# Kernel tuning notes

Measured on AMD Instinct MI355X. Metric: run time of the kernel, lower is better.

## Reference

```python
import jax, jax.numpy as jnp
import numpy as np

MAT_MODE = ((0, 1), (0, 2), (1, 2))
VEC_MODE = (2, 1, 0)


def _bilinear2d(feat, xy):
    # feat [C,H,W]; xy [N,2] in [-1,1], x indexes W, y indexes H (align_corners=True)
    C, H, W = feat.shape
    x = jnp.clip((xy[:, 0] + 1.0) * 0.5 * (W - 1), 0.0, W - 1)
    y = jnp.clip((xy[:, 1] + 1.0) * 0.5 * (H - 1), 0.0, H - 1)
    x0 = jnp.floor(x).astype(jnp.int32)
    y0 = jnp.floor(y).astype(jnp.int32)
    x1 = jnp.minimum(x0 + 1, W - 1)
    y1 = jnp.minimum(y0 + 1, H - 1)
    wx = (x - x0)[None, :]
    wy = (y - y0)[None, :]
    f00 = feat[:, y0, x0]
    f01 = feat[:, y0, x1]
    f10 = feat[:, y1, x0]
    f11 = feat[:, y1, x1]
    top = f00 * (1.0 - wx) + f01 * wx
    bot = f10 * (1.0 - wx) + f11 * wx
    return top * (1.0 - wy) + bot * wy  # [C,N]


def _linear1d(feat, z):
    # feat [C,L]; z [N] in [-1,1] (align_corners=True); x-coord of grid_sample is 0 (width=1)
    C, L = feat.shape
    y = jnp.clip((z + 1.0) * 0.5 * (L - 1), 0.0, L - 1)
    y0 = jnp.floor(y).astype(jnp.int32)
    y1 = jnp.minimum(y0 + 1, L - 1)
    wy = (y - y0)[None, :]
    return feat[:, y0] * (1.0 - wy) + feat[:, y1] * wy  # [C,N]


def _skew(w):
    # w [N,3] -> [N,3,3]
    z = jnp.zeros_like(w[:, 0])
    return jnp.stack([
        jnp.stack([z, -w[:, 2], w[:, 1]], -1),
        jnp.stack([w[:, 2], z, -w[:, 0]], -1),
        jnp.stack([-w[:, 1], w[:, 0], z], -1),
    ], axis=1)


def _sample_bwfield(planes, lines, xn):
    # planes [3,6,16,H,W], lines [3,6,16,L], xn [N,3] normalized -> bwf [N,6]
    N = xn.shape[0]
    bwf = jnp.zeros((6, N), dtype=xn.dtype)
    for p in range(3):
        m0, m1 = MAT_MODE[p]
        xy = jnp.stack([xn[:, m0], xn[:, m1]], axis=-1)  # [N,2]
        S, C, H, W = planes[p].shape  # 6,16,H,W
        psamp = _bilinear2d(planes[p].reshape(S * C, H, W), xy).reshape(S, C, N)
        lsamp = _linear1d(lines[p].reshape(S * C, -1), xn[:, VEC_MODE[p]]).reshape(S, C, N)
        bwf = bwf + jnp.sum(psamp * lsamp, axis=1)  # [6,N]
    return bwf.T  # [N,6]


def _warp(xyz, viewdirs, planes, lines, ray_aabb):
    shape = xyz.shape
    pts = xyz.reshape(-1, 3)
    inv = 2.0 / (ray_aabb[1] - ray_aabb[0])
    xn = (pts - ray_aabb[0]) * inv - 1.0
    bwf = _sample_bwfield(planes, lines, xn)  # [N,6]
    w, v = bwf[:, :3], bwf[:, 3:]
    theta = jnp.sqrt(jnp.clip(jnp.sum(w * w, axis=-1), 1e-6, None))  # [N]
    w = w / theta[:, None]
    v = v / theta[:, None]
    Wm = _skew(w)                                   # [N,3,3]
    W2 = jnp.einsum('nij,njk->nik', Wm, Wm)
    s = jnp.sin(theta)[:, None, None]
    c = jnp.cos(theta)[:, None, None]
    th = theta[:, None, None]
    I = jnp.eye(3, dtype=xyz.dtype)
    R = I + s * Wm + (1.0 - c) * W2                 # exp_so3
    P = th * I + (1.0 - c) * Wm + (th - s) * W2     # V(theta)
    t = jnp.einsum('nij,nj->ni', P, v)              # translation
    xw = jnp.einsum('nij,nj->ni', R, pts) + t
    vw = jnp.einsum('nij,nj->ni', R, viewdirs.reshape(-1, 3))
    return xw.reshape(shape), vw.reshape(shape)


def setup_inputs() -> dict:
    key = jax.random.key(0)
    k1, k2, k3, k4 = jax.random.split(key, 4)
    n_rays, n_samp = 2048, 256
    G = 128
    xyz = jax.random.uniform(k1, (n_rays, n_samp, 3), jnp.float32, -1.4, 1.4)
    vd = jax.random.normal(k2, (n_rays, n_samp, 3), jnp.float32)
    vd = vd / jnp.linalg.norm(vd, axis=-1, keepdims=True)
    planes = 0.1 * jax.random.normal(k3, (3, 6, 16, G, G), jnp.float32)
    lines = 0.1 * jax.random.normal(k4, (3, 6, 16, G), jnp.float32)
    ray_aabb = jnp.array([[-1.5, -1.5, -1.5], [1.5, 1.5, 1.5]], jnp.float32)
    transforms = jnp.zeros((4, 4), jnp.float32)
    ray_valid = jnp.ones((n_rays, n_samp), bool)
    return {"xyz_sampled": xyz, "viewdirs": vd, "transforms": transforms,
            "ray_valid": ray_valid, "planes": planes, "lines": lines,
            "ray_aabb": ray_aabb}


def reference(xyz_sampled, viewdirs, transforms, ray_valid, planes, lines, ray_aabb):
    # transforms and ray_valid are accepted but unused by Map_BWCaster.forward
    return _warp(xyz_sampled, viewdirs, planes, lines, ray_aabb)
```

## Files before the change

kernel.cpp:

```cpp
#include <hip/hip_runtime.h>
#include <cstdint>
#include <cstddef>

#define GRES 128
#define SC   96

typedef float v2f __attribute__((ext_vector_type(2)));

template<bool HI>
__device__ __forceinline__ v2f cvt2(uint32_t q)
{
    return __builtin_amdgcn_cvt_pk_f32_fp8(q, HI);
}

__device__ __forceinline__ uint32_t u4w(const uint4& q, int c)
{
    return c == 0 ? q.x : c == 1 ? q.y : c == 2 ? q.z : q.w;
}

#define NPLANE_T (3 * 12 * GRES * GRES)
#define NLINE_T  (3 * 12 * GRES)

__global__ __launch_bounds__(256) void tp_split(const float* __restrict__ planes,
                                                const float* __restrict__ lines,
                                                uint8_t* __restrict__ A,
                                                uint8_t* __restrict__ B,
                                                uint8_t* __restrict__ L)
{
    int t = blockIdx.x * 256 + threadIdx.x;
    if (t < NPLANE_T) {
        int xy = t & (GRES * GRES - 1);
        int pg = t >> 14;
        int g  = pg % 12;
        int p  = pg / 12;
        int ch0 = 8 * g;
        const float* src = planes + ((size_t)(p * SC + ch0) * (GRES * GRES)) + xy;
        float v[8];
        #pragma unroll
        for (int i = 0; i < 8; ++i) v[i] = src[(size_t)i * (GRES * GRES)];
        uint32_t w0 = 0, w1 = 0;
        w0 = __builtin_amdgcn_cvt_pk_fp8_f32(v[0], v[1], w0, false);
        w0 = __builtin_amdgcn_cvt_pk_fp8_f32(v[2], v[3], w0, true);
        w1 = __builtin_amdgcn_cvt_pk_fp8_f32(v[4], v[5], w1, false);
        w1 = __builtin_amdgcn_cvt_pk_fp8_f32(v[6], v[7], w1, true);
        uint2 pkt = make_uint2(w0, w1);
        int texel = (p << 14) + xy;
        if (g < 8)
            *(uint2*)(A + (size_t)texel * 64 + 8 * g) = pkt;
        else
            *(uint2*)(B + (size_t)texel * 32 + 8 * (g - 8)) = pkt;
    } else if (t < NPLANE_T + NLINE_T) {
        int r = t - NPLANE_T;
        int z  = r & (GRES - 1);
        int pg = r >> 7;
        int g  = pg % 12;
        int p  = pg / 12;
        int ch0 = 8 * g;
        const float* src = lines + ((size_t)(p * SC + ch0) * GRES) + z;
        float v[8];
        #pragma unroll
        for (int i = 0; i < 8; ++i) v[i] = src[(size_t)i * GRES];
        uint32_t w0 = 0, w1 = 0;
        w0 = __builtin_amdgcn_cvt_pk_fp8_f32(v[0], v[1], w0, false);
        w0 = __builtin_amdgcn_cvt_pk_fp8_f32(v[2], v[3], w0, true);
        w1 = __builtin_amdgcn_cvt_pk_fp8_f32(v[4], v[5], w1, false);
        w1 = __builtin_amdgcn_cvt_pk_fp8_f32(v[6], v[7], w1, true);
        *(uint2*)(L + (size_t)(p * GRES + z) * 128 + 8 * g) = make_uint2(w0, w1);
    }
}

__device__ __forceinline__ void axis_setup(float xnv, int& i0, int& i1, float& w)
{
    float f = (xnv + 1.0f) * 0.5f * (float)(GRES - 1);
    f = fminf(fmaxf(f, 0.0f), (float)(GRES - 1));
    float ff = floorf(f);
    i0 = (int)ff;
    i1 = min(i0 + 1, GRES - 1);
    w  = f - ff;
}

__global__ __launch_bounds__(256) void bwcast_s4(
    const float* __restrict__ xyz, const float* __restrict__ vdirs,
    const uint8_t* __restrict__ A, const uint8_t* __restrict__ B,
    const uint8_t* __restrict__ L, const float* __restrict__ aabb,
    float* __restrict__ out, int N)
{
    int t = blockIdx.x * 256 + threadIdx.x;
    int n = t >> 2;
    int l = t & 3;
    if (n >= N) return;
    int lane = threadIdx.x & 63;

    float px = xyz[3 * n + 0], py = xyz[3 * n + 1], pz = xyz[3 * n + 2];
    float xn[3];
    xn[0] = (px - aabb[0]) * (2.0f / (aabb[3] - aabb[0])) - 1.0f;
    xn[1] = (py - aabb[1]) * (2.0f / (aabb[4] - aabb[1])) - 1.0f;
    xn[2] = (pz - aabb[2]) * (2.0f / (aabb[5] - aabb[2])) - 1.0f;

    uint32_t aoff[3][4], boff[3][4];
    uint32_t lo4[3][2], lo2[3][2];
    float W[3][4], UZ[3], WZ[3];

    #pragma unroll
    for (int p = 0; p < 3; ++p) {
        constexpr int M0[3] = {0, 0, 1};
        constexpr int M1[3] = {1, 2, 2};
        constexpr int MV[3] = {2, 1, 0};
        int x0, x1, y0, y1, z0, z1;
        float wx, wy, wz;
        axis_setup(xn[M0[p]], x0, x1, wx);
        axis_setup(xn[M1[p]], y0, y1, wy);
        axis_setup(xn[MV[p]], z0, z1, wz);
        uint32_t t00 = (uint32_t)((p * GRES + y0) * GRES + x0);
        uint32_t t01 = (uint32_t)((p * GRES + y0) * GRES + x1);
        uint32_t t10 = (uint32_t)((p * GRES + y1) * GRES + x0);
        uint32_t t11 = (uint32_t)((p * GRES + y1) * GRES + x1);
        uint32_t a16 = (uint32_t)l * 16u, b8 = (uint32_t)l * 8u;
        aoff[p][0] = t00 * 64u + a16;  boff[p][0] = t00 * 32u + b8;
        aoff[p][1] = t01 * 64u + a16;  boff[p][1] = t01 * 32u + b8;
        aoff[p][2] = t10 * 64u + a16;  boff[p][2] = t10 * 32u + b8;
        aoff[p][3] = t11 * 64u + a16;  boff[p][3] = t11 * 32u + b8;
        uint32_t r0 = (uint32_t)(p * GRES + z0) * 128u;
        uint32_t r1 = (uint32_t)(p * GRES + z1) * 128u;
        lo4[p][0] = r0 + a16;          lo2[p][0] = r0 + 64u + b8;
        lo4[p][1] = r1 + a16;          lo2[p][1] = r1 + 64u + b8;
        W[p][0] = (1.f - wx) * (1.f - wy);
        W[p][1] = wx * (1.f - wy);
        W[p][2] = (1.f - wx) * wy;
        W[p][3] = wx * wy;
        UZ[p] = 1.f - wz;
        WZ[p] = wz;
    }

    v2f aLE = (v2f)(0.f), aLO = (v2f)(0.f);
    v2f aHE = (v2f)(0.f), aHO = (v2f)(0.f);

    #pragma unroll
    for (int p = 0; p < 3; ++p) {
        uint4 a4[4]; uint2 b2[4];
        #pragma unroll
        for (int c = 0; c < 4; ++c) {
            a4[c] = *(const uint4*)(A + aoff[p][c]);
            b2[c] = *(const uint2*)(B + boff[p][c]);
        }
        uint4 l4[2]; uint2 l2[2];
        #pragma unroll
        for (int d = 0; d < 2; ++d) {
            l4[d] = *(const uint4*)(L + lo4[p][d]);
            l2[d] = *(const uint2*)(L + lo2[p][d]);
        }
        v2f w0v = (v2f)(W[p][0]);
        v2f w1v = (v2f)(W[p][1]);
        v2f w2v = (v2f)(W[p][2]);
        v2f w3v = (v2f)(W[p][3]);
        v2f uzv = (v2f)(UZ[p]);
        v2f wzv = (v2f)(WZ[p]);

        #pragma unroll
        for (int k = 0; k < 4; ++k) {
            uint32_t wa0 = u4w(a4[0], k), wa1 = u4w(a4[1], k);
            uint32_t wa2 = u4w(a4[2], k), wa3 = u4w(a4[3], k);
            uint32_t wl0 = u4w(l4[0], k), wl1 = u4w(l4[1], k);
            v2f pv = cvt2<false>(wa0) * w0v;
            pv = cvt2<false>(wa1) * w1v + pv;
            pv = cvt2<false>(wa2) * w2v + pv;
            pv = cvt2<false>(wa3) * w3v + pv;
            v2f lv = cvt2<false>(wl1) * wzv;
            lv = cvt2<false>(wl0) * uzv + lv;
            aLE = pv * lv + aLE;
            v2f pu = cvt2<true>(wa0) * w0v;
            pu = cvt2<true>(wa1) * w1v + pu;
            pu = cvt2<true>(wa2) * w2v + pu;
            pu = cvt2<true>(wa3) * w3v + pu;
            v2f lu = cvt2<true>(wl1) * wzv;
            lu = cvt2<true>(wl0) * uzv + lu;
            aLO = pu * lu + aLO;
        }
        #pragma unroll
        for (int k = 0; k < 2; ++k) {
            uint32_t wb0 = k ? b2[0].y : b2[0].x;
            uint32_t wb1 = k ? b2[1].y : b2[1].x;
            uint32_t wb2 = k ? b2[2].y : b2[2].x;
            uint32_t wb3 = k ? b2[3].y : b2[3].x;
            uint32_t wl0 = k ? l2[0].y : l2[0].x;
            uint32_t wl1 = k ? l2[1].y : l2[1].x;
            v2f pv = cvt2<false>(wb0) * w0v;
            pv = cvt2<false>(wb1) * w1v + pv;
            pv = cvt2<false>(wb2) * w2v + pv;
            pv = cvt2<false>(wb3) * w3v + pv;
            v2f lv = cvt2<false>(wl1) * wzv;
            lv = cvt2<false>(wl0) * uzv + lv;
            aHE = pv * lv + aHE;
            v2f pu = cvt2<true>(wb0) * w0v;
            pu = cvt2<true>(wb1) * w1v + pu;
            pu = cvt2<true>(wb2) * w2v + pu;
            pu = cvt2<true>(wb3) * w3v + pu;
            v2f lu = cvt2<true>(wl1) * wzv;
            lu = cvt2<true>(wl0) * uzv + lu;
            aHO = pu * lu + aHO;
        }
    }

    v2f sl = aLE + aLO;
    float part_lo = sl[0] + sl[1];
    v2f sh = aHE + aHO;
    float part_hi = sh[0] + sh[1];

    int base = lane & ~3;
    float bw[6];
    bw[0] = __shfl(part_lo, base + 0);
    bw[1] = __shfl(part_lo, base + 1);
    bw[2] = __shfl(part_lo, base + 2);
    bw[3] = __shfl(part_lo, base + 3);
    float ph2 = part_hi + __shfl_xor(part_hi, 1);
    bw[4] = __shfl(ph2, base + 0);
    bw[5] = __shfl(ph2, base + 2);

    float wxr = bw[0], wyr = bw[1], wzr = bw[2];
    float dotw = wxr * wxr + wyr * wyr + wzr * wzr;
    float theta = sqrtf(fmaxf(dotw, 1e-6f));
    float it = 1.0f / theta;
    float ux = wxr * it, uy = wyr * it, un = wzr * it;
    float vx = bw[3] * it, vy = bw[4] * it, vz = bw[5] * it;
    float st, ct;
    sincosf(theta, &st, &ct);
    float q   = ux * ux + uy * uy + un * un;
    float omc = 1.0f - ct;
    float ra = 1.0f - omc * q;
    float R00 = ra + omc * ux * ux;
    float R01 = omc * ux * uy - st * un;
    float R02 = omc * ux * un + st * uy;
    float R10 = omc * uy * ux + st * un;
    float R11 = ra + omc * uy * uy;
    float R12 = omc * uy * un - st * ux;
    float R20 = omc * un * ux - st * uy;
    float R21 = omc * un * uy + st * ux;
    float R22 = ra + omc * un * un;
    float tms = theta - st;
    float pa  = theta - tms * q;
    float P00 = pa + tms * ux * ux;
    float P01 = tms * ux * uy - omc * un;
    float P02 = tms * ux * un + omc * uy;
    float P10 = tms * uy * ux + omc * un;
    float P11 = pa + tms * uy * uy;
    float P12 = tms * uy * un - omc * ux;
    float P20 = tms * un * ux - omc * uy;
    float P21 = tms * un * uy + omc * ux;
    float P22 = pa + tms * un * un;

    float tx = P00 * vx + P01 * vy + P02 * vz;
    float ty = P10 * vx + P11 * vy + P12 * vz;
    float tz = P20 * vx + P21 * vy + P22 * vz;

    float ox = R00 * px + R01 * py + R02 * pz + tx;
    float oy = R10 * px + R11 * py + R12 * pz + ty;
    float oz = R20 * px + R21 * py + R22 * pz + tz;

    float dx = vdirs[3 * n + 0], dy = vdirs[3 * n + 1], dz = vdirs[3 * n + 2];
    float wvx = R00 * dx + R01 * dy + R02 * dz;
    float wvy = R10 * dx + R11 * dy + R12 * dz;
    float wvz = R20 * dx + R21 * dy + R22 * dz;

    if (l < 3) {
        float o  = (l == 0) ? ox : (l == 1) ? oy : oz;
        float wv = (l == 0) ? wvx : (l == 1) ? wvy : wvz;
        out[3 * n + l] = o;
        out[(size_t)3 * N + 3 * n + l] = wv;
    }
}

__global__ __launch_bounds__(256) void bwcast_direct(
    const float* __restrict__ xyz, const float* __restrict__ vdirs,
    const float* __restrict__ PL, const float* __restrict__ LN,
    const float* __restrict__ aabb, float* __restrict__ out, int N)
{
    int n = blockIdx.x * 256 + threadIdx.x;
    if (n >= N) return;

    float px = xyz[3 * n + 0], py = xyz[3 * n + 1], pz = xyz[3 * n + 2];
    float xn[3];
    xn[0] = (px - aabb[0]) * (2.0f / (aabb[3] - aabb[0])) - 1.0f;
    xn[1] = (py - aabb[1]) * (2.0f / (aabb[4] - aabb[1])) - 1.0f;
    xn[2] = (pz - aabb[2]) * (2.0f / (aabb[5] - aabb[2])) - 1.0f;

    float bw[6] = {0.f, 0.f, 0.f, 0.f, 0.f, 0.f};

    #pragma unroll
    for (int p = 0; p < 3; ++p) {
        constexpr int M0[3] = {0, 0, 1};
        constexpr int M1[3] = {1, 2, 2};
        constexpr int MV[3] = {2, 1, 0};
        int x0, x1, y0, y1, z0, z1;
        float wx, wy, wz;
        axis_setup(xn[M0[p]], x0, x1, wx);
        axis_setup(xn[M1[p]], y0, y1, wy);
        axis_setup(xn[MV[p]], z0, z1, wz);
        float w00 = (1.f - wx) * (1.f - wy);
        float w01 = wx * (1.f - wy);
        float w10 = (1.f - wx) * wy;
        float w11 = wx * wy;
        float uz = 1.f - wz;
        #pragma unroll
        for (int s = 0; s < 6; ++s) {
            float acc = bw[s];
            for (int c = 0; c < 16; ++c) {
                int sc = s * 16 + c;
                const float* pb = PL + (size_t)(p * SC + sc) * (GRES * GRES);
                float f00 = pb[y0 * GRES + x0];
                float f01 = pb[y0 * GRES + x1];
                float f10 = pb[y1 * GRES + x0];
                float f11 = pb[y1 * GRES + x1];
                const float* lb = LN + (size_t)(p * SC + sc) * GRES;
                float lv = fmaf(lb[z0], uz, lb[z1] * wz);
                float pv = fmaf(f00, w00, fmaf(f01, w01, fmaf(f10, w10, f11 * w11)));
                acc = fmaf(pv, lv, acc);
            }
            bw[s] = acc;
        }
    }

    float wxr = bw[0], wyr = bw[1], wzr = bw[2];
    float dotw = wxr * wxr + wyr * wyr + wzr * wzr;
    float theta = sqrtf(fmaxf(dotw, 1e-6f));
    float it = 1.0f / theta;
    float ux = wxr * it, uy = wyr * it, un = wzr * it;
    float vx = bw[3] * it, vy = bw[4] * it, vz = bw[5] * it;
    float st, ct;
    sincosf(theta, &st, &ct);
    float q   = ux * ux + uy * uy + un * un;
    float omc = 1.0f - ct;
    float ra = 1.0f - omc * q;
    float R00 = ra + omc * ux * ux;
    float R01 = omc * ux * uy - st * un;
    float R02 = omc * ux * un + st * uy;
    float R10 = omc * uy * ux + st * un;
    float R11 = ra + omc * uy * uy;
    float R12 = omc * uy * un - st * ux;
    float R20 = omc * un * ux - st * uy;
    float R21 = omc * un * uy + st * ux;
    float R22 = ra + omc * un * un;
    float tms = theta - st;
    float pa  = theta - tms * q;
    float P00 = pa + tms * ux * ux;
    float P01 = tms * ux * uy - omc * un;
    float P02 = tms * ux * un + omc * uy;
    float P10 = tms * uy * ux + omc * un;
    float P11 = pa + tms * uy * uy;
    float P12 = tms * uy * un - omc * ux;
    float P20 = tms * un * ux - omc * uy;
    float P21 = tms * un * uy + omc * ux;
    float P22 = pa + tms * un * un;

    float tx = P00 * vx + P01 * vy + P02 * vz;
    float ty = P10 * vx + P11 * vy + P12 * vz;
    float tz = P20 * vx + P21 * vy + P22 * vz;

    out[3 * n + 0] = R00 * px + R01 * py + R02 * pz + tx;
    out[3 * n + 1] = R10 * px + R11 * py + R12 * pz + ty;
    out[3 * n + 2] = R20 * px + R21 * py + R22 * pz + tz;

    float dx = vdirs[3 * n + 0], dy = vdirs[3 * n + 1], dz = vdirs[3 * n + 2];
    size_t off = (size_t)3 * N;
    out[off + 3 * n + 0] = R00 * dx + R01 * dy + R02 * dz;
    out[off + 3 * n + 1] = R10 * dx + R11 * dy + R12 * dz;
    out[off + 3 * n + 2] = R20 * dx + R21 * dy + R22 * dz;
}

extern "C" void kernel_launch(void* const* d_in, const int* in_sizes, int n_in,
                              void* d_out, int out_size, void* d_ws, size_t ws_size,
                              hipStream_t stream)
{
    const float* xyz    = (const float*)d_in[0];
    const float* vd     = (const float*)d_in[1];
    const float* planes = (const float*)d_in[4];
    const float* lines  = (const float*)d_in[5];
    const float* aabb   = (const float*)d_in[6];
    float* out = (float*)d_out;

    int N = in_sizes[0] / 3;

    size_t szA = (size_t)3 * GRES * GRES * 64;
    size_t szB = (size_t)3 * GRES * GRES * 32;
    size_t szL = (size_t)3 * GRES * 128;

    if (ws_size >= szA + szB + szL) {
        uint8_t* A = (uint8_t*)d_ws;
        uint8_t* Bp = A + szA;
        uint8_t* L = Bp + szB;
        int tp_threads = NPLANE_T + NLINE_T;
        tp_split<<<(tp_threads + 255) / 256, 256, 0, stream>>>(planes, lines, A, Bp, L);
        int threads = N * 4;
        bwcast_s4<<<(threads + 255) / 256, 256, 0, stream>>>(
            xyz, vd, A, Bp, L, aabb, out, N);
    } else {
        bwcast_direct<<<(N + 255) / 256, 256, 0, stream>>>(xyz, vd, planes, lines, aabb, out, N);
    }
}
```

Before: 155.5 us.

## Split each point across two lanes instead of four with wider fp8 loads

Each sample point is now handled by two threads instead of four, and each thread loads 32 bytes of A, 16 of B, and matching line bytes per corner. The six bw components are exchanged with three xor-shuffles, and each lane writes one of the two outputs. Accurate sincosf is replaced by __sinf/__cosf. This halves the thread count and the redundant per-point setup and epilogue math, at the cost of more registers per thread and possibly lower occupancy and memory-level parallelism.

Measured after the change: 181.5 us. +16.8%, slower.

```diff
diff --git a/kernel.cpp b/kernel.cpp
--- a/kernel.cpp
+++ b/kernel.cpp
@@ -79,17 +79,38 @@
     w  = f - ff;
 }
 
-__global__ __launch_bounds__(256) void bwcast_s4(
+__device__ __forceinline__ void word_fma(
+    uint32_t wa0, uint32_t wa1, uint32_t wa2, uint32_t wa3,
+    uint32_t wl0, uint32_t wl1,
+    v2f w0v, v2f w1v, v2f w2v, v2f w3v, v2f uzv, v2f wzv,
+    v2f& accE, v2f& accO)
+{
+    v2f pv = cvt2<false>(wa0) * w0v;
+    pv = cvt2<false>(wa1) * w1v + pv;
+    pv = cvt2<false>(wa2) * w2v + pv;
+    pv = cvt2<false>(wa3) * w3v + pv;
+    v2f lv = cvt2<false>(wl1) * wzv;
+    lv = cvt2<false>(wl0) * uzv + lv;
+    accE = pv * lv + accE;
+    v2f pu = cvt2<true>(wa0) * w0v;
+    pu = cvt2<true>(wa1) * w1v + pu;
+    pu = cvt2<true>(wa2) * w2v + pu;
+    pu = cvt2<true>(wa3) * w3v + pu;
+    v2f lu = cvt2<true>(wl1) * wzv;
+    lu = cvt2<true>(wl0) * uzv + lu;
+    accO = pu * lu + accO;
+}
+
+__global__ __launch_bounds__(256) void bwcast_d2(
     const float* __restrict__ xyz, const float* __restrict__ vdirs,
     const uint8_t* __restrict__ A, const uint8_t* __restrict__ B,
     const uint8_t* __restrict__ L, const float* __restrict__ aabb,
     float* __restrict__ out, int N)
 {
     int t = blockIdx.x * 256 + threadIdx.x;
-    int n = t >> 2;
-    int l = t & 3;
+    int n = t >> 1;
+    int h = t & 1;
     if (n >= N) return;
-    int lane = threadIdx.x & 63;
 
     float px = xyz[3 * n + 0], py = xyz[3 * n + 1], pz = xyz[3 * n + 2];
     float xn[3];
@@ -97,9 +118,12 @@
     xn[1] = (py - aabb[1]) * (2.0f / (aabb[4] - aabb[1])) - 1.0f;
     xn[2] = (pz - aabb[2]) * (2.0f / (aabb[5] - aabb[2])) - 1.0f;
 
-    uint32_t aoff[3][4], boff[3][4];
-    uint32_t lo4[3][2], lo2[3][2];
-    float W[3][4], UZ[3], WZ[3];
+    const uint32_t a32 = (uint32_t)h * 32u;
+    const uint32_t b16 = (uint32_t)h * 16u;
+
+    v2f acA0E = (v2f)(0.f), acA0O = (v2f)(0.f);
+    v2f acA1E = (v2f)(0.f), acA1O = (v2f)(0.f);
+    v2f acBE  = (v2f)(0.f), acBO  = (v2f)(0.f);
 
     #pragma unroll
     for (int p = 0; p < 3; ++p) {
@@ -111,110 +135,168 @@
         axis_setup(xn[M0[p]], x0, x1, wx);
         axis_setup(xn[M1[p]], y0, y1, wy);
         axis_setup(xn[MV[p]], z0, z1, wz);
-        uint32_t t00 = (uint32_t)((p * GRES + y0) * GRES + x0);
-        uint32_t t01 = (uint32_t)((p * GRES + y0) * GRES + x1);
-        uint32_t t10 = (uint32_t)((p * GRES + y1) * GRES + x0);
-        uint32_t t11 = (uint32_t)((p * GRES + y1) * GRES + x1);
-        uint32_t a16 = (uint32_t)l * 16u, b8 = (uint32_t)l * 8u;
-        aoff[p][0] = t00 * 64u + a16;  boff[p][0] = t00 * 32u + b8;
-        aoff[p][1] = t01 * 64u + a16;  boff[p][1] = t01 * 32u + b8;
-        aoff[p][2] = t10 * 64u + a16;  boff[p][2] = t10 * 32u + b8;
-        aoff[p][3] = t11 * 64u + a16;  boff[p][3] = t11 * 32u + b8;
+        uint32_t tex[4];
+        tex[0] = (uint32_t)((p * GRES + y0) * GRES + x0);
+        tex[1] = (uint32_t)((p * GRES + y0) * GRES + x1);
+        tex[2] = (uint32_t)((p * GRES + y1) * GRES + x0);
+        tex[3] = (uint32_t)((p * GRES + y1) * GRES + x1);
         uint32_t r0 = (uint32_t)(p * GRES + z0) * 128u;
         uint32_t r1 = (uint32_t)(p * GRES + z1) * 128u;
-        lo4[p][0] = r0 + a16;          lo2[p][0] = r0 + 64u + b8;
-        lo4[p][1] = r1 + a16;          lo2[p][1] = r1 + 64u + b8;
-        W[p][0] = (1.f - wx) * (1.f - wy);
-        W[p][1] = wx * (1.f - wy);
-        W[p][2] = (1.f - wx) * wy;
-        W[p][3] = wx * wy;
-        UZ[p] = 1.f - wz;
-        WZ[p] = wz;
-    }
-
-    v2f aLE = (v2f)(0.f), aLO = (v2f)(0.f);
-    v2f aHE = (v2f)(0.f), aHO = (v2f)(0.f);
+
+        uint4 a0[4], a1[4], b4[4];
+        #pragma unroll
+        for (int c = 0; c < 4; ++c) {
+            const uint8_t* ab = A + (size_t)tex[c] * 64u + a32;
+            a0[c] = *(const uint4*)(ab);
+            a1[c] = *(const uint4*)(ab + 16);
+            b4[c] = *(const uint4*)(B + (size_t)tex[c] * 32u + b16);
+        }
+        uint4 l0A0 = *(const uint4*)(L + r0 + a32);
+        uint4 l0A1 = *(const uint4*)(L + r0 + a32 + 16);
+        uint4 l0B  = *(const uint4*)(L + r0 + 64u + b16);
+        uint4 l1A0 = *(const uint4*)(L + r1 + a32);
+        uint4 l1A1 = *(const uint4*)(L + r1 + a32 + 16);
+        uint4 l1B  = *(const uint4*)(L + r1 + 64u + b16);
+
+        v2f w0v = (v2f)((1.f - wx) * (1.f - wy));
+        v2f w1v = (v2f)(wx * (1.f - wy));
+        v2f w2v = (v2f)((1.f - wx) * wy);
+        v2f w3v = (v2f)(wx * wy);
+        v2f uzv = (v2f)(1.f - wz);
+        v2f wzv = (v2f)(wz);
+
+        #pragma unroll
+        for (int w = 0; w < 4; ++w)
+            word_fma(u4w(a0[0], w), u4w(a0[1], w), u4w(a0[2], w), u4w(a0[3], w),
+                     u4w(l0A0, w), u4w(l1A0, w),
+                     w0v, w1v, w2v, w3v, uzv, wzv, acA0E, acA0O);
+        #pragma unroll
+        for (int w = 0; w < 4; ++w)
+            word_fma(u4w(a1[0], w), u4w(a1[1], w), u4w(a1[2], w), u4w(a1[3], w),
+                     u4w(l0A1, w), u4w(l1A1, w),
+                     w0v, w1v, w2v, w3v, uzv, wzv, acA1E, acA1O);
+        #pragma unroll
+        for (int w = 0; w < 4; ++w)
+            word_fma(u4w(b4[0], w), u4w(b4[1], w), u4w(b4[2], w), u4w(b4[3], w),
+                     u4w(l0B, w), u4w(l1B, w),
+                     w0v, w1v, w2v, w3v, uzv, wzv, acBE, acBO);
+    }
+
+    v2f sA0 = acA0E + acA0O;
+    v2f sA1 = acA1E + acA1O;
+    v2f sB  = acBE + acBO;
+    float pA0 = sA0[0] + sA0[1];
+    float pA1 = sA1[0] + sA1[1];
+    float pB  = sB[0] + sB[1];
+
+    float oA0 = __shfl_xor(pA0, 1);
+    float oA1 = __shfl_xor(pA1, 1);
+    float oB  = __shfl_xor(pB, 1);
+    float bw[6];
+    bw[0] = h ? oA0 : pA0;
+    bw[1] = h ? oA1 : pA1;
+    bw[2] = h ? pA0 : oA0;
+    bw[3] = h ? pA1 : oA1;
+    bw[4] = h ? oB  : pB;
+    bw[5] = h ? pB  : oB;
+
+    float wxr = bw[0], wyr = bw[1], wzr = bw[2];
+    float dotw = wxr * wxr + wyr * wyr + wzr * wzr;
+    float theta = sqrtf(fmaxf(dotw, 1e-6f));
+    float it = 1.0f / theta;
+    float ux = wxr * it, uy = wyr * it, un = wzr * it;
+    float vx = bw[3] * it, vy = bw[4] * it, vz = bw[5] * it;
+    float st = __sinf(theta);
+    float ct = __cosf(theta);
+    float q   = ux * ux + uy * uy + un * un;
+    float omc = 1.0f - ct;
+    float ra = 1.0f - omc * q;
+    float R00 = ra + omc * ux * ux;
+    float R01 = omc * ux * uy - st * un;
+    float R02 = omc * ux * un + st * uy;
+    float R10 = omc * uy * ux + st * un;
+    float R11 = ra + omc * uy * uy;
+    float R12 = omc * uy * un - st * ux;
+    float R20 = omc * un * ux - st * uy;
+    float R21 = omc * un * uy + st * ux;
+    float R22 = ra + omc * un * un;
+    float tms = theta - st;
+    float pa  = theta - tms * q;
+    float P00 = pa + tms * ux * ux;
+    float P01 = tms * ux * uy - omc * un;
+    float P02 = tms * ux * un + omc * uy;
+    float P10 = tms * uy * ux + omc * un;
+    float P11 = pa + tms * uy * uy;
+    float P12 = tms * uy * un - omc * ux;
+    float P20 = tms * un * ux - omc * uy;
+    float P21 = tms * un * uy + omc * ux;
+    float P22 = pa + tms * un * un;
+
+    if (h == 0) {
+        float tx = P00 * vx + P01 * vy + P02 * vz;
+        float ty = P10 * vx + P11 * vy + P12 * vz;
+        float tz = P20 * vx + P21 * vy + P22 * vz;
+        out[3 * n + 0] = R00 * px + R01 * py + R02 * pz + tx;
+        out[3 * n + 1] = R10 * px + R11 * py + R12 * pz + ty;
+        out[3 * n + 2] = R20 * px + R21 * py + R22 * pz + tz;
+    } else {
+        float dx = vdirs[3 * n + 0], dy = vdirs[3 * n + 1], dz = vdirs[3 * n + 2];
+        size_t off = (size_t)3 * N;
+        out[off + 3 * n + 0] = R00 * dx + R01 * dy + R02 * dz;
+        out[off + 3 * n + 1] = R10 * dx + R11 * dy + R12 * dz;
+        out[off + 3 * n + 2] = R20 * dx + R21 * dy + R22 * dz;
+    }
+}
+
+__global__ __launch_bounds__(256) void bwcast_direct(
+    const float* __restrict__ xyz, const float* __restrict__ vdirs,
+    const float* __restrict__ PL, const float* __restrict__ LN,
+    const float* __restrict__ aabb, float* __restrict__ out, int N)
+{
+    int n = blockIdx.x * 256 + threadIdx.x;
+    if (n >= N) return;
+
+    float px = xyz[3 * n + 0], py = xyz[3 * n + 1], pz = xyz[3 * n + 2];
+    float xn[3];
+    xn[0] = (px - aabb[0]) * (2.0f / (aabb[3] - aabb[0])) - 1.0f;
+    xn[1] = (py - aabb[1]) * (2.0f / (aabb[4] - aabb[1])) - 1.0f;
+    xn[2] = (pz - aabb[2]) * (2.0f / (aabb[5] - aabb[2])) - 1.0f;
+
+    float bw[6] = {0.f, 0.f, 0.f, 0.f, 0.f, 0.f};
 
     #pragma unroll
     for (int p = 0; p < 3; ++p) {
-        uint4 a4[4]; uint2 b2[4];
-        #pragma unroll
-        for (int c = 0; c < 4; ++c) {
-            a4[c] = *(const uint4*)(A + aoff[p][c]);
-            b2[c] = *(const uint2*)(B + boff[p][c]);
+        constexpr int M0[3] = {0, 0, 1};
+        constexpr int M1[3] = {1, 2, 2};
+        constexpr int MV[3] = {2, 1, 0};
+        int x0, x1, y0, y1, z0, z1;
+        float wx, wy, wz;
+        axis_setup(xn[M0[p]], x0, x1, wx);
+        axis_setup(xn[M1[p]], y0, y1, wy);
+        axis_setup(xn[MV[p]], z0, z1, wz);
+        float w00 = (1.f - wx) * (1.f - wy);
+        float w01 = wx * (1.f - wy);
+        float w10 = (1.f - wx) * wy;
+        float w11 = wx * wy;
+        float uz = 1.f - wz;
+        #pragma unroll
+        for (int s = 0; s < 6; ++s) {
+            float acc = bw[s];
+            for (int c = 0; c < 16; ++c) {
+                int sc = s * 16 + c;
+                const float* pb = PL + (size_t)(p * SC + sc) * (GRES * GRES);
+                float f00 = pb[y0 * GRES + x0];
+                float f01 = pb[y0 * GRES + x1];
+                float f10 = pb[y1 * GRES + x0];
+                float f11 = pb[y1 * GRES + x1];
+                const float* lb = LN + (size_t)(p * SC + sc) * GRES;
+                float lv = fmaf(lb[z0], uz, lb[z1] * wz);
+                float pv = fmaf(f00, w00, fmaf(f01, w01, fmaf(f10, w10, f11 * w11)));
+                acc = fmaf(pv, lv, acc);
+            }
+            bw[s] = acc;
         }
-        uint4 l4[2]; uint2 l2[2];
-        #pragma unroll
-        for (int d = 0; d < 2; ++d) {
-            l4[d] = *(const uint4*)(L + lo4[p][d]);
-            l2[d] = *(const uint2*)(L + lo2[p][d]);
-        }
-        v2f w0v = (v2f)(W[p][0]);
-        v2f w1v = (v2f)(W[p][1]);
-        v2f w2v = (v2f)(W[p][2]);
-        v2f w3v = (v2f)(W[p][3]);
-        v2f uzv = (v2f)(UZ[p]);
-        v2f wzv = (v2f)(WZ[p]);
-
-        #pragma unroll
-        for (int k = 0; k < 4; ++k) {
-            uint32_t wa0 = u4w(a4[0], k), wa1 = u4w(a4[1], k);
-            uint32_t wa2 = u4w(a4[2], k), wa3 = u4w(a4[3], k);
-            uint32_t wl0 = u4w(l4[0], k), wl1 = u4w(l4[1], k);
-            v2f pv = cvt2<false>(wa0) * w0v;
-            pv = cvt2<false>(wa1) * w1v + pv;
-            pv = cvt2<false>(wa2) * w2v + pv;
-            pv = cvt2<false>(wa3) * w3v + pv;
-            v2f lv = cvt2<false>(wl1) * wzv;
-            lv = cvt2<false>(wl0) * uzv + lv;
-            aLE = pv * lv + aLE;
-            v2f pu = cvt2<true>(wa0) * w0v;
-            pu = cvt2<true>(wa1) * w1v + pu;
-            pu = cvt2<true>(wa2) * w2v + pu;
-            pu = cvt2<true>(wa3) * w3v + pu;
-            v2f lu = cvt2<true>(wl1) * wzv;
-            lu = cvt2<true>(wl0) * uzv + lu;
-            aLO = pu * lu + aLO;
-        }
-        #pragma unroll
-        for (int k = 0; k < 2; ++k) {
-            uint32_t wb0 = k ? b2[0].y : b2[0].x;
-            uint32_t wb1 = k ? b2[1].y : b2[1].x;
-            uint32_t wb2 = k ? b2[2].y : b2[2].x;
-            uint32_t wb3 = k ? b2[3].y : b2[3].x;
-            uint32_t wl0 = k ? l2[0].y : l2[0].x;
-            uint32_t wl1 = k ? l2[1].y : l2[1].x;
-            v2f pv = cvt2<false>(wb0) * w0v;
-            pv = cvt2<false>(wb1) * w1v + pv;
-            pv = cvt2<false>(wb2) * w2v + pv;
-            pv = cvt2<false>(wb3) * w3v + pv;
-            v2f lv = cvt2<false>(wl1) * wzv;
-            lv = cvt2<false>(wl0) * uzv + lv;
-            aHE = pv * lv + aHE;
-            v2f pu = cvt2<true>(wb0) * w0v;
-            pu = cvt2<true>(wb1) * w1v + pu;
-            pu = cvt2<true>(wb2) * w2v + pu;
-            pu = cvt2<true>(wb3) * w3v + pu;
-            v2f lu = cvt2<true>(wl1) * wzv;
-            lu = cvt2<true>(wl0) * uzv + lu;
-            aHO = pu * lu + aHO;
-        }
-    }
-
-    v2f sl = aLE + aLO;
-    float part_lo = sl[0] + sl[1];
-    v2f sh = aHE + aHO;
-    float part_hi = sh[0] + sh[1];
-
-    int base = lane & ~3;
-    float bw[6];
-    bw[0] = __shfl(part_lo, base + 0);
-    bw[1] = __shfl(part_lo, base + 1);
-    bw[2] = __shfl(part_lo, base + 2);
-    bw[3] = __shfl(part_lo, base + 3);
-    float ph2 = part_hi + __shfl_xor(part_hi, 1);
-    bw[4] = __shfl(ph2, base + 0);
-    bw[5] = __shfl(ph2, base + 2);
+    }
 
     float wxr = bw[0], wyr = bw[1], wzr = bw[2];
     float dotw = wxr * wxr + wyr * wyr + wzr * wzr;
@@ -252,109 +334,6 @@
     float ty = P10 * vx + P11 * vy + P12 * vz;
     float tz = P20 * vx + P21 * vy + P22 * vz;
 
-    float ox = R00 * px + R01 * py + R02 * pz + tx;
-    float oy = R10 * px + R11 * py + R12 * pz + ty;
-    float oz = R20 * px + R21 * py + R22 * pz + tz;
-
-    float dx = vdirs[3 * n + 0], dy = vdirs[3 * n + 1], dz = vdirs[3 * n + 2];
-    float wvx = R00 * dx + R01 * dy + R02 * dz;
-    float wvy = R10 * dx + R11 * dy + R12 * dz;
-    float wvz = R20 * dx + R21 * dy + R22 * dz;
-
-    if (l < 3) {
-        float o  = (l == 0) ? ox : (l == 1) ? oy : oz;
-        float wv = (l == 0) ? wvx : (l == 1) ? wvy : wvz;
-        out[3 * n + l] = o;
-        out[(size_t)3 * N + 3 * n + l] = wv;
-    }
-}
-
-__global__ __launch_bounds__(256) void bwcast_direct(
-    const float* __restrict__ xyz, const float* __restrict__ vdirs,
-    const float* __restrict__ PL, const float* __restrict__ LN,
-    const float* __restrict__ aabb, float* __restrict__ out, int N)
-{
-    int n = blockIdx.x * 256 + threadIdx.x;
-    if (n >= N) return;
-
-    float px = xyz[3 * n + 0], py = xyz[3 * n + 1], pz = xyz[3 * n + 2];
-    float xn[3];
-    xn[0] = (px - aabb[0]) * (2.0f / (aabb[3] - aabb[0])) - 1.0f;
-    xn[1] = (py - aabb[1]) * (2.0f / (aabb[4] - aabb[1])) - 1.0f;
-    xn[2] = (pz - aabb[2]) * (2.0f / (aabb[5] - aabb[2])) - 1.0f;
-
-    float bw[6] = {0.f, 0.f, 0.f, 0.f, 0.f, 0.f};
-
-    #pragma unroll
-    for (int p = 0; p < 3; ++p) {
-        constexpr int M0[3] = {0, 0, 1};
-        constexpr int M1[3] = {1, 2, 2};
-        constexpr int MV[3] = {2, 1, 0};
-        int x0, x1, y0, y1, z0, z1;
-        float wx, wy, wz;
-        axis_setup(xn[M0[p]], x0, x1, wx);
-        axis_setup(xn[M1[p]], y0, y1, wy);
-        axis_setup(xn[MV[p]], z0, z1, wz);
-        float w00 = (1.f - wx) * (1.f - wy);
-        float w01 = wx * (1.f - wy);
-        float w10 = (1.f - wx) * wy;
-        float w11 = wx * wy;
-        float uz = 1.f - wz;
-        #pragma unroll
-        for (int s = 0; s < 6; ++s) {
-            float acc = bw[s];
-            for (int c = 0; c < 16; ++c) {
-                int sc = s * 16 + c;
-                const float* pb = PL + (size_t)(p * SC + sc) * (GRES * GRES);
-                float f00 = pb[y0 * GRES + x0];
-                float f01 = pb[y0 * GRES + x1];
-                float f10 = pb[y1 * GRES + x0];
-                float f11 = pb[y1 * GRES + x1];
-                const float* lb = LN + (size_t)(p * SC + sc) * GRES;
-                float lv = fmaf(lb[z0], uz, lb[z1] * wz);
-                float pv = fmaf(f00, w00, fmaf(f01, w01, fmaf(f10, w10, f11 * w11)));
-                acc = fmaf(pv, lv, acc);
-            }
-            bw[s] = acc;
-        }
-    }
-
-    float wxr = bw[0], wyr = bw[1], wzr = bw[2];
-    float dotw = wxr * wxr + wyr * wyr + wzr * wzr;
-    float theta = sqrtf(fmaxf(dotw, 1e-6f));
-    float it = 1.0f / theta;
-    float ux = wxr * it, uy = wyr * it, un = wzr * it;
-    float vx = bw[3] * it, vy = bw[4] * it, vz = bw[5] * it;
-    float st, ct;
-    sincosf(theta, &st, &ct);
-    float q   = ux * ux + uy * uy + un * un;
-    float omc = 1.0f - ct;
-    float ra = 1.0f - omc * q;
-    float R00 = ra + omc * ux * ux;
-    float R01 = omc * ux * uy - st * un;
-    float R02 = omc * ux * un + st * uy;
-    float R10 = omc * uy * ux + st * un;
-    float R11 = ra + omc * uy * uy;
-    float R12 = omc * uy * un - st * ux;
-    float R20 = omc * un * ux - st * uy;
-    float R21 = omc * un * uy + st * ux;
-    float R22 = ra + omc * un * un;
-    float tms = theta - st;
-    float pa  = theta - tms * q;
-    float P00 = pa + tms * ux * ux;
-    float P01 = tms * ux * uy - omc * un;
-    float P02 = tms * ux * un + omc * uy;
-    float P10 = tms * uy * ux + omc * un;
-    float P11 = pa + tms * uy * uy;
-    float P12 = tms * uy * un - omc * ux;
-    float P20 = tms * un * ux - omc * uy;
-    float P21 = tms * un * uy + omc * ux;
-    float P22 = pa + tms * un * un;
-
-    float tx = P00 * vx + P01 * vy + P02 * vz;
-    float ty = P10 * vx + P11 * vy + P12 * vz;
-    float tz = P20 * vx + P21 * vy + P22 * vz;
-
     out[3 * n + 0] = R00 * px + R01 * py + R02 * pz + tx;
     out[3 * n + 1] = R10 * px + R11 * py + R12 * pz + ty;
     out[3 * n + 2] = R20 * px + R21 * py + R22 * pz + tz;
@@ -389,8 +368,8 @@
         uint8_t* L = Bp + szB;
         int tp_threads = NPLANE_T + NLINE_T;
         tp_split<<<(tp_threads + 255) / 256, 256, 0, stream>>>(planes, lines, A, Bp, L);
-        int threads = N * 4;
-        bwcast_s4<<<(threads + 255) / 256, 256, 0, stream>>>(
+        int threads = N * 2;
+        bwcast_d2<<<(threads + 255) / 256, 256, 0, stream>>>(
             xyz, vd, A, Bp, L, aabb, out, N);
     } else {
         bwcast_direct<<<(N + 255) / 256, 256, 0, stream>>>(xyz, vd, planes, lines, aabb, out, N);
```
